# Performance work log

Hardware: AMD Instinct MI355X
Metric: run time of the kernel (lower is better)

The kernel has to match this reference:

```python
import jax, jax.numpy as jnp
import numpy as np

# SorscherRNN constants. NOTE: AdaptationRNN.__init__ swaps the names:
# self.beta = alpha_kwarg, self.alpha = beta_kwarg. We replicate the effective math:
#   z  = v_t @ W_ih.T + h @ W_hh.T - ALPHA_KW * v_adapt
#   v_adapt = v_adapt + BETA_KW * (z_prev - v_adapt)   (z_prev is the PREVIOUS post-subtraction z)
ALPHA_KW = 0.1  # used as the subtraction coefficient (self.beta)
BETA_KW = 0.9   # used as the adaptation rate (self.alpha)
NG, NP = 4096, 512
B, T = 64, 100


def setup_inputs() -> dict:
    key = jax.random.key(0)
    ks = jax.random.split(key, 6)
    def xavier(k, shape):
        fan_out, fan_in = shape
        a = jnp.sqrt(6.0 / (fan_in + fan_out))
        return jax.random.uniform(k, shape, jnp.float32, -a, a)
    return {
        "v": jax.random.normal(ks[0], (B, T, 2), jnp.float32),
        "p0": jax.random.uniform(ks[1], (B, NP), jnp.float32),
        "W_init": xavier(ks[2], (NG, NP)),  # init_position_encoder weight [Ng, Np]
        "W_ih": xavier(ks[3], (NG, 2)),     # RNN input weight W
        "W_hh": xavier(ks[4], (NG, NG)),    # RNN recurrent weight Wh
        "W_dec": xavier(ks[5], (NP, NG)),   # decoder weight [Np, Ng]
    }


def _sorscher_forward(v, p0, W_init, W_ih, W_hh, W_dec):
    h0 = p0 @ W_init.T                       # [B, Ng]
    va0 = jnp.zeros_like(h0)
    zp0 = jnp.zeros_like(h0)

    def step(carry, v_t):
        h, va, zp = carry
        z = v_t @ W_ih.T + h @ W_hh.T        # [B, Ng]
        z = z - ALPHA_KW * va                # z -= self.beta * v (old v)
        va = va + BETA_KW * (zp - va)        # v += self.alpha * (z_prev - v)
        s = jax.nn.relu(z)
        return (s, va, z), s                 # z_prev is post-subtraction z

    v_t_first = jnp.transpose(v, (1, 0, 2))  # [T, B, 2]
    _, g = jax.lax.scan(step, (h0, va0, zp0), v_t_first)
    g = jnp.transpose(g, (1, 0, 2))          # [B, T, Ng]
    return g @ W_dec.T                       # place_preds [B, T, Np] (log_softmax=False)


def reference(v, p0, W_init, W_ih, W_hh, W_dec):
    return _sorscher_forward(v, p0, W_init, W_ih, W_hh, W_dec)
```

## Files before the change

### kernel.cpp

```cpp
#include <hip/hip_runtime.h>
#include <hip/hip_bf16.h>

#define NG 4096
#define NP 512
#define TT 100
#define NCOL 4608
#define NKS 8

typedef __bf16  bf16x8 __attribute__((ext_vector_type(8)));
typedef float   f32x4  __attribute__((ext_vector_type(4)));
typedef __hip_bfloat16 bf;
typedef unsigned short u16;

#define ALPHA_BF 0.10009765625f
#define BETA_BF  0.8984375f

__device__ __forceinline__ bf16x8 ldfrag(const bf* p) {
  return *reinterpret_cast<const bf16x8*>(p);
}
__device__ __forceinline__ f32x4 mfma16(bf16x8 a, bf16x8 b, f32x4 c) {
  return __builtin_amdgcn_mfma_f32_16x16x32_bf16(a, b, c, 0, 0, 0);
}
__device__ __forceinline__ float ldin(const void* p, long i, int isf) {
  return isf ? ((const float*)p)[i] : __bfloat162float(((const bf*)p)[i]);
}
__device__ __forceinline__ float bfr(float x) {
  return __bfloat162float(__float2bfloat16(x));
}
__device__ __forceinline__ long qidx(int m, int c) {
  int kk = c >> 5, qd = (c >> 3) & 3, j = c & 7;
  int mt = m >> 4, lm = m & 15;
  return (((long)kk * 4 + mt) * 64 + (qd * 16 + lm)) * 8 + j;
}

__global__ void probe_kernel(const u16* __restrict__ w, int* __restrict__ flag) {
  int lane = threadIdx.x;
  int okall = 1, cntb = 0;
#pragma unroll
  for (int j = 0; j < 4; ++j) {
    u16 x = w[2 * (lane * 4 + j)];
    int e = (x >> 7) & 0xFF;
    int bok = (e >= 60 && e <= 126);
    int zok = (e == 0);
    okall &= (bok | zok);
    cntb += bok;
  }
  unsigned long long b1 = __ballot(okall != 0);
  unsigned long long b2 = __ballot(cntb >= 3);
  if (lane == 0)
    *flag = (b1 == ~0ull && __popcll(b2) >= 48) ? 0 : 1;
}

__global__ __launch_bounds__(256) void cvt_pack_kernel(
    const void* __restrict__ Whh, const void* __restrict__ Wdec,
    bf* __restrict__ PH, bf* __restrict__ PL,
    const int* __restrict__ flag) {
  int isf = *flag;
  long n = (long)NCOL * NG;
  long i = (long)blockIdx.x * 256 + threadIdx.x;
  long stride = (long)gridDim.x * 256;
  for (; i < n; i += stride) {
    int j    = (int)(i & 7);
    int lane = (int)((i >> 3) & 63);
    int kk   = (int)((i >> 9) & 127);
    int strip= (int)(i >> 16);
    int col  = strip * 16 + (lane & 15);
    int k    = kk * 32 + (lane >> 4) * 8 + j;
    long src = (col < NG) ? ((long)col * NG + k)
                          : ((long)(col - NG) * NG + k);
    const void* W = (col < NG) ? Whh : Wdec;
    float x = ldin(W, src, isf);
    bf h = __float2bfloat16(x);
    PH[i] = h;
    PL[i] = __float2bfloat16(isf ? (x - __bfloat162float(h)) : 0.f);
  }
}

__global__ __launch_bounds__(256) void init_kernel(
    const void* __restrict__ p0, const void* __restrict__ Winit,
    const int* __restrict__ flag,
    bf* __restrict__ hi0, bf* __restrict__ lo0,
    float* __restrict__ va, float* __restrict__ zp)
{
  int isf = *flag;
  int tid = blockIdx.x * 256 + threadIdx.x;
  int b = tid >> 12;
  int n = tid & 4095;
  float acc = 0.f;
  if (isf) {
    const float* pp = (const float*)p0 + (long)b * NP;
    const float* pw = (const float*)Winit + (long)n * NP;
#pragma unroll 4
    for (int k = 0; k < NP; k += 4) {
      float4 a = *(const float4*)(pp + k);
      float4 w = *(const float4*)(pw + k);
      acc += a.x * w.x + a.y * w.y + a.z * w.z + a.w * w.w;
    }
  } else {
    const bf* pp = (const bf*)p0 + (long)b * NP;
    const bf* pw = (const bf*)Winit + (long)n * NP;
#pragma unroll 4
    for (int k = 0; k < NP; k += 8) {
      bf16x8 a = ldfrag(pp + k);
      bf16x8 w = ldfrag(pw + k);
#pragma unroll
      for (int j = 0; j < 8; ++j) acc += (float)a[j] * (float)w[j];
    }
  }
  bf h = __float2bfloat16(acc);
  float lo = isf ? (acc - __bfloat162float(h)) : 0.f;
  long q = qidx(b, n);
  hi0[q] = h;
  lo0[q] = __float2bfloat16(lo);
  long idx = (long)b * NG + n;
  va[idx] = 0.f;
  zp[idx] = 0.f;
}

__global__ __launch_bounds__(256) void s1_kernel(
    const bf* __restrict__ Qh, const bf* __restrict__ Ql,
    float* __restrict__ part,
    const bf* __restrict__ PH, const bf* __restrict__ PL,
    const int* __restrict__ flag, int t)
{
  int ct = blockIdx.x >> 3;
  int ks = blockIdx.x & 7;
  bool isdec = (ct >= 64);
  if (isdec ? (t == 0) : (t == TT)) return;

  int isf = *flag;
  int tid  = threadIdx.x;
  int wave = tid >> 6;
  int lane = tid & 63;
  int quad = lane >> 4, l16 = lane & 15;
  int strip = ct * 4 + wave;

  const bf* pBh = PH + ((long)strip * 128 + ks * 16) * 512 + lane * 8;
  const bf* pBl = PL + ((long)strip * 128 + ks * 16) * 512 + lane * 8;
  const bf* pAh = Qh + (long)ks * 32768 + lane * 8;
  const bf* pAl = Ql + (long)ks * 32768 + lane * 8;

  f32x4 acc0 = {0.f,0.f,0.f,0.f}, acc1 = acc0, acc2 = acc0, acc3 = acc0;
  if (isf) {
#pragma unroll 4
    for (int i = 0; i < 16; ++i) {
      const bf* ah = pAh + i * 2048;
      const bf* al = pAl + i * 2048;
      bf16x8 bh = ldfrag(pBh + i * 512);
      bf16x8 bl = ldfrag(pBl + i * 512);
      bf16x8 a0 = ldfrag(ah);
      bf16x8 a1 = ldfrag(ah + 512);
      bf16x8 a2 = ldfrag(ah + 1024);
      bf16x8 a3 = ldfrag(ah + 1536);
      bf16x8 l0 = ldfrag(al);
      bf16x8 l1 = ldfrag(al + 512);
      bf16x8 l2 = ldfrag(al + 1024);
      bf16x8 l3 = ldfrag(al + 1536);
      acc0 = mfma16(a0, bh, acc0); acc0 = mfma16(l0, bh, acc0); acc0 = mfma16(a0, bl, acc0);
      acc1 = mfma16(a1, bh, acc1); acc1 = mfma16(l1, bh, acc1); acc1 = mfma16(a1, bl, acc1);
      acc2 = mfma16(a2, bh, acc2); acc2 = mfma16(l2, bh, acc2); acc2 = mfma16(a2, bl, acc2);
      acc3 = mfma16(a3, bh, acc3); acc3 = mfma16(l3, bh, acc3); acc3 = mfma16(a3, bl, acc3);
    }
  } else {
#pragma unroll 4
    for (int i = 0; i < 16; ++i) {
      const bf* ah = pAh + i * 2048;
      bf16x8 bh = ldfrag(pBh + i * 512);
      acc0 = mfma16(ldfrag(ah),        bh, acc0);
      acc1 = mfma16(ldfrag(ah + 512),  bh, acc1);
      acc2 = mfma16(ldfrag(ah + 1024), bh, acc2);
      acc3 = mfma16(ldfrag(ah + 1536), bh, acc3);
    }
  }

  float* pp = part + ((long)ks * 64 + quad * 4) * NCOL + strip * 16 + l16;
#pragma unroll
  for (int mt = 0; mt < 4; ++mt) {
    f32x4 a = (mt == 0) ? acc0 : (mt == 1) ? acc1 : (mt == 2) ? acc2 : acc3;
#pragma unroll
    for (int r = 0; r < 4; ++r)
      pp[((long)mt * 16 + r) * NCOL] = a[r];
  }
}

__global__ __launch_bounds__(256) void s2_kernel(
    const float* __restrict__ part,
    bf* __restrict__ hN, bf* __restrict__ lN,
    float* __restrict__ va, float* __restrict__ zp,
    const void* __restrict__ Wih, const void* __restrict__ v,
    const int* __restrict__ flag, void* __restrict__ out, int t)
{
  int isf = *flag;
#pragma unroll
  for (int i = 0; i < 4; ++i) {
    int e = blockIdx.x * 1024 + i * 256 + threadIdx.x;
    int m = e / NCOL;
    int c = e - m * NCOL;
    bool dcol = (c >= NG);
    if (dcol ? (t == 0) : (t == TT)) continue;

    float z = 0.f;
#pragma unroll
    for (int js = 0; js < NKS; ++js)
      z += part[((long)js * 64 + m) * NCOL + c];

    if (dcol) {
      long o = ((long)m * TT + (t - 1)) * NP + (c - NG);
      if (isf) ((float*)out)[o] = z;
      else     ((bf*)out)[o]    = __float2bfloat16(z);
      continue;
    }

    float w0 = ldin(Wih, 2L * c, isf);
    float w1 = ldin(Wih, 2L * c + 1, isf);
    float v0 = ldin(v, ((long)m * TT + t) * 2, isf);
    float v1 = ldin(v, ((long)m * TT + t) * 2 + 1, isf);

    long idx = (long)m * NG + c;
    float vao = va[idx], zpo = zp[idx];
    float s;
    if (isf) {
      z += v0 * w0 + v1 * w1;
      z -= 0.1f * vao;
      va[idx] = vao + 0.9f * (zpo - vao);
      zp[idx] = z;
      s = fmaxf(z, 0.f);
      bf sh = __float2bfloat16(s);
      long q = qidx(m, c);
      hN[q] = sh;
      lN[q] = __float2bfloat16(s - __bfloat162float(sh));
    } else {
      float zmm = bfr(z);
      float zv  = bfr(v0 * w0 + v1 * w1);
      float z0  = bfr(zmm + zv);
      float sub = bfr(ALPHA_BF * vao);
      float z1  = bfr(z0 - sub);
      float d   = bfr(zpo - vao);
      float mm  = bfr(BETA_BF * d);
      va[idx]   = bfr(vao + mm);
      zp[idx]   = z1;
      s = fmaxf(z1, 0.f);
      long q = qidx(m, c);
      hN[q] = __float2bfloat16(s);
      lN[q] = __float2bfloat16(0.f);
    }
  }
}

extern "C" void kernel_launch(void* const* d_in, const int* in_sizes, int n_in,
                              void* d_out, int out_size, void* d_ws, size_t ws_size,
                              hipStream_t stream) {
  const void* v     = d_in[0];
  const void* p0    = d_in[1];
  const void* Winit = d_in[2];
  const void* Wih   = d_in[3];
  const void* Whh   = d_in[4];
  const void* Wdec  = d_in[5];

  size_t off = 0;
  char* w = (char*)d_ws;
  int*   flag = (int*)(w + off);          off += 64;
  bf*    PH   = (bf*)(w + off);           off += (size_t)NCOL * NG * 2;
  bf*    PL   = (bf*)(w + off);           off += (size_t)NCOL * NG * 2;
  bf* hi0 = (bf*)(w + off);               off += (size_t)64 * NG * 2;
  bf* hi1 = (bf*)(w + off);               off += (size_t)64 * NG * 2;
  bf* lo0 = (bf*)(w + off);               off += (size_t)64 * NG * 2;
  bf* lo1 = (bf*)(w + off);               off += (size_t)64 * NG * 2;
  float* va   = (float*)(w + off);        off += (size_t)64 * NG * 4;
  float* zp   = (float*)(w + off);        off += (size_t)64 * NG * 4;
  float* part = (float*)(w + off);        off += (size_t)NKS * 64 * NCOL * 4;

  if (ws_size < off) return;

  probe_kernel<<<1, 64, 0, stream>>>((const u16*)Whh, flag);
  cvt_pack_kernel<<<8192, 256, 0, stream>>>(Whh, Wdec, PH, PL, flag);
  init_kernel<<<1024, 256, 0, stream>>>(p0, Winit, flag, hi0, lo0, va, zp);

  bf* hbuf[2] = { hi0, hi1 };
  bf* lbuf[2] = { lo0, lo1 };
  for (int t = 0; t <= TT; ++t) {
    s1_kernel<<<576, 256, 0, stream>>>(hbuf[t & 1], lbuf[t & 1], part,
                                       PH, PL, flag, t);
    s2_kernel<<<288, 256, 0, stream>>>(part, hbuf[(t + 1) & 1],
                                       lbuf[(t + 1) & 1], va, zp,
                                       Wih, v, flag, d_out, t);
  }
}
```

Baseline: 2.882 ms.

## Fuse split-K matmul and recurrence update into one kernel with LDS reduction

Merges the per-step s1 (split-K MFMA partial products to global memory) and s2 (reduction plus recurrence update) kernels into a single 512-thread kernel. Each block now handles one 16-column strip and half the batch, with 8 waves covering the K splits, and reduces the partials through shared memory instead of a global buffer. This halves the per-step launch count and removes the global partial-sum round trip, but each wave now computes only two M tiles, so B fragments are reused less. The weight packing kernel is also vectorised to 8 elements per thread, and the init GEMV is restructured to use wave-level shuffle reductions.

```diff
diff --git a/kernel.cpp b/kernel.cpp
--- a/kernel.cpp
+++ b/kernel.cpp
@@ -56,23 +56,35 @@
     bf* __restrict__ PH, bf* __restrict__ PL,
     const int* __restrict__ flag) {
   int isf = *flag;
-  long n = (long)NCOL * NG;
+  long n8 = (long)NCOL * NG / 8;
   long i = (long)blockIdx.x * 256 + threadIdx.x;
   long stride = (long)gridDim.x * 256;
-  for (; i < n; i += stride) {
-    int j    = (int)(i & 7);
-    int lane = (int)((i >> 3) & 63);
-    int kk   = (int)((i >> 9) & 127);
-    int strip= (int)(i >> 16);
+  for (; i < n8; i += stride) {
+    int lane = (int)(i & 63);
+    int kk   = (int)((i >> 6) & 127);
+    int strip= (int)(i >> 13);
     int col  = strip * 16 + (lane & 15);
-    int k    = kk * 32 + (lane >> 4) * 8 + j;
-    long src = (col < NG) ? ((long)col * NG + k)
-                          : ((long)(col - NG) * NG + k);
+    int k0   = kk * 32 + (lane >> 4) * 8;
     const void* W = (col < NG) ? Whh : Wdec;
-    float x = ldin(W, src, isf);
-    bf h = __float2bfloat16(x);
-    PH[i] = h;
-    PL[i] = __float2bfloat16(isf ? (x - __bfloat162float(h)) : 0.f);
+    long src = (long)((col < NG) ? col : col - NG) * NG + k0;
+    if (isf) {
+      const float* ps = (const float*)W + src;
+      float4 x = *(const float4*)ps, y = *(const float4*)(ps + 4);
+      float xs[8] = {x.x, x.y, x.z, x.w, y.x, y.y, y.z, y.w};
+      bf16x8 h, l;
+#pragma unroll
+      for (int j = 0; j < 8; ++j) {
+        bf hh = __float2bfloat16(xs[j]);
+        bf ll = __float2bfloat16(xs[j] - __bfloat162float(hh));
+        h[j] = *reinterpret_cast<__bf16*>(&hh);
+        l[j] = *reinterpret_cast<__bf16*>(&ll);
+      }
+      *reinterpret_cast<bf16x8*>(PH + i * 8) = h;
+      *reinterpret_cast<bf16x8*>(PL + i * 8) = l;
+    } else {
+      *reinterpret_cast<bf16x8*>(PH + i * 8) =
+          *reinterpret_cast<const bf16x8*>((const bf*)W + src);
+    }
   }
 }
 
@@ -83,166 +95,151 @@
     float* __restrict__ va, float* __restrict__ zp)
 {
   int isf = *flag;
-  int tid = blockIdx.x * 256 + threadIdx.x;
-  int b = tid >> 12;
-  int n = tid & 4095;
-  float acc = 0.f;
+  int g = blockIdx.x * 4 + (threadIdx.x >> 6);
+  int lane = threadIdx.x & 63;
+  int b  = g >> 7;
+  int n0 = g & 127;
+  float pf[8];
   if (isf) {
-    const float* pp = (const float*)p0 + (long)b * NP;
-    const float* pw = (const float*)Winit + (long)n * NP;
-#pragma unroll 4
-    for (int k = 0; k < NP; k += 4) {
-      float4 a = *(const float4*)(pp + k);
-      float4 w = *(const float4*)(pw + k);
-      acc += a.x * w.x + a.y * w.y + a.z * w.z + a.w * w.w;
-    }
+    const float* pp = (const float*)p0 + (long)b * NP + lane * 8;
+    float4 x = *(const float4*)pp, y = *(const float4*)(pp + 4);
+    pf[0]=x.x; pf[1]=x.y; pf[2]=x.z; pf[3]=x.w;
+    pf[4]=y.x; pf[5]=y.y; pf[6]=y.z; pf[7]=y.w;
   } else {
-    const bf* pp = (const bf*)p0 + (long)b * NP;
-    const bf* pw = (const bf*)Winit + (long)n * NP;
-#pragma unroll 4
-    for (int k = 0; k < NP; k += 8) {
-      bf16x8 a = ldfrag(pp + k);
-      bf16x8 w = ldfrag(pw + k);
-#pragma unroll
-      for (int j = 0; j < 8; ++j) acc += (float)a[j] * (float)w[j];
-    }
-  }
-  bf h = __float2bfloat16(acc);
-  float lo = isf ? (acc - __bfloat162float(h)) : 0.f;
-  long q = qidx(b, n);
-  hi0[q] = h;
-  lo0[q] = __float2bfloat16(lo);
-  long idx = (long)b * NG + n;
-  va[idx] = 0.f;
-  zp[idx] = 0.f;
-}
-
-__global__ __launch_bounds__(256) void s1_kernel(
+    bf16x8 a = ldfrag((const bf*)p0 + (long)b * NP + lane * 8);
+#pragma unroll
+    for (int j = 0; j < 8; ++j) pf[j] = (float)a[j];
+  }
+  for (int it = 0; it < 32; ++it) {
+    int n = n0 + (it << 7);
+    float acc;
+    if (isf) {
+      const float* pw = (const float*)Winit + (long)n * NP + lane * 8;
+      float4 x = *(const float4*)pw, y = *(const float4*)(pw + 4);
+      acc = pf[0]*x.x + pf[1]*x.y + pf[2]*x.z + pf[3]*x.w
+          + pf[4]*y.x + pf[5]*y.y + pf[6]*y.z + pf[7]*y.w;
+    } else {
+      bf16x8 wv = ldfrag((const bf*)Winit + (long)n * NP + lane * 8);
+      acc = 0.f;
+#pragma unroll
+      for (int j = 0; j < 8; ++j) acc += pf[j] * (float)wv[j];
+    }
+#pragma unroll
+    for (int s = 32; s >= 1; s >>= 1) acc += __shfl_xor(acc, s, 64);
+    if (lane == 0) {
+      bf h = __float2bfloat16(acc);
+      float lo = isf ? (acc - __bfloat162float(h)) : 0.f;
+      long q = qidx(b, n);
+      hi0[q] = h;
+      lo0[q] = __float2bfloat16(lo);
+      long idx = (long)b * NG + n;
+      va[idx] = 0.f;
+      zp[idx] = 0.f;
+    }
+  }
+}
+
+__global__ __launch_bounds__(512, 4) void s12_kernel(
     const bf* __restrict__ Qh, const bf* __restrict__ Ql,
-    float* __restrict__ part,
+    bf* __restrict__ hN, bf* __restrict__ lN,
+    float* __restrict__ va, float* __restrict__ zp,
     const bf* __restrict__ PH, const bf* __restrict__ PL,
-    const int* __restrict__ flag, int t)
+    const void* __restrict__ Wih, const void* __restrict__ vin,
+    const int* __restrict__ flag, void* __restrict__ out, int t)
 {
-  int ct = blockIdx.x >> 3;
-  int ks = blockIdx.x & 7;
-  bool isdec = (ct >= 64);
+  int strip = blockIdx.x >> 1;
+  int mh    = blockIdx.x & 1;
+  bool isdec = (strip >= 256);
   if (isdec ? (t == 0) : (t == TT)) return;
 
   int isf = *flag;
-  int tid  = threadIdx.x;
-  int wave = tid >> 6;
+  int tid = threadIdx.x;
+  int ks   = tid >> 6;
   int lane = tid & 63;
   int quad = lane >> 4, l16 = lane & 15;
-  int strip = ct * 4 + wave;
 
   const bf* pBh = PH + ((long)strip * 128 + ks * 16) * 512 + lane * 8;
-  const bf* pBl = PL + ((long)strip * 128 + ks * 16) * 512 + lane * 8;
-  const bf* pAh = Qh + (long)ks * 32768 + lane * 8;
-  const bf* pAl = Ql + (long)ks * 32768 + lane * 8;
-
-  f32x4 acc0 = {0.f,0.f,0.f,0.f}, acc1 = acc0, acc2 = acc0, acc3 = acc0;
+  const bf* pAh = Qh + (long)ks * 32768 + mh * 1024 + lane * 8;
+
+  f32x4 acc0 = {0.f,0.f,0.f,0.f}, acc1 = acc0;
   if (isf) {
+    const bf* pBl = PL + ((long)strip * 128 + ks * 16) * 512 + lane * 8;
+    const bf* pAl = Ql + (long)ks * 32768 + mh * 1024 + lane * 8;
 #pragma unroll 4
     for (int i = 0; i < 16; ++i) {
+      bf16x8 bh = ldfrag(pBh + i * 512);
+      bf16x8 bl = ldfrag(pBl + i * 512);
       const bf* ah = pAh + i * 2048;
       const bf* al = pAl + i * 2048;
-      bf16x8 bh = ldfrag(pBh + i * 512);
-      bf16x8 bl = ldfrag(pBl + i * 512);
-      bf16x8 a0 = ldfrag(ah);
-      bf16x8 a1 = ldfrag(ah + 512);
-      bf16x8 a2 = ldfrag(ah + 1024);
-      bf16x8 a3 = ldfrag(ah + 1536);
-      bf16x8 l0 = ldfrag(al);
-      bf16x8 l1 = ldfrag(al + 512);
-      bf16x8 l2 = ldfrag(al + 1024);
-      bf16x8 l3 = ldfrag(al + 1536);
+      bf16x8 a0 = ldfrag(ah),       a1 = ldfrag(ah + 512);
+      bf16x8 l0 = ldfrag(al),       l1 = ldfrag(al + 512);
       acc0 = mfma16(a0, bh, acc0); acc0 = mfma16(l0, bh, acc0); acc0 = mfma16(a0, bl, acc0);
       acc1 = mfma16(a1, bh, acc1); acc1 = mfma16(l1, bh, acc1); acc1 = mfma16(a1, bl, acc1);
-      acc2 = mfma16(a2, bh, acc2); acc2 = mfma16(l2, bh, acc2); acc2 = mfma16(a2, bl, acc2);
-      acc3 = mfma16(a3, bh, acc3); acc3 = mfma16(l3, bh, acc3); acc3 = mfma16(a3, bl, acc3);
     }
   } else {
 #pragma unroll 4
     for (int i = 0; i < 16; ++i) {
+      bf16x8 bh = ldfrag(pBh + i * 512);
       const bf* ah = pAh + i * 2048;
-      bf16x8 bh = ldfrag(pBh + i * 512);
-      acc0 = mfma16(ldfrag(ah),        bh, acc0);
-      acc1 = mfma16(ldfrag(ah + 512),  bh, acc1);
-      acc2 = mfma16(ldfrag(ah + 1024), bh, acc2);
-      acc3 = mfma16(ldfrag(ah + 1536), bh, acc3);
-    }
-  }
-
-  float* pp = part + ((long)ks * 64 + quad * 4) * NCOL + strip * 16 + l16;
-#pragma unroll
-  for (int mt = 0; mt < 4; ++mt) {
-    f32x4 a = (mt == 0) ? acc0 : (mt == 1) ? acc1 : (mt == 2) ? acc2 : acc3;
-#pragma unroll
-    for (int r = 0; r < 4; ++r)
-      pp[((long)mt * 16 + r) * NCOL] = a[r];
-  }
-}
-
-__global__ __launch_bounds__(256) void s2_kernel(
-    const float* __restrict__ part,
-    bf* __restrict__ hN, bf* __restrict__ lN,
-    float* __restrict__ va, float* __restrict__ zp,
-    const void* __restrict__ Wih, const void* __restrict__ v,
-    const int* __restrict__ flag, void* __restrict__ out, int t)
-{
-  int isf = *flag;
-#pragma unroll
-  for (int i = 0; i < 4; ++i) {
-    int e = blockIdx.x * 1024 + i * 256 + threadIdx.x;
-    int m = e / NCOL;
-    int c = e - m * NCOL;
-    bool dcol = (c >= NG);
-    if (dcol ? (t == 0) : (t == TT)) continue;
-
+      acc0 = mfma16(ldfrag(ah),       bh, acc0);
+      acc1 = mfma16(ldfrag(ah + 512), bh, acc1);
+    }
+  }
+
+  __shared__ float red[NKS][32][16];
+#pragma unroll
+  for (int r = 0; r < 4; ++r) {
+    red[ks][quad * 4 + r][l16]      = acc0[r];
+    red[ks][16 + quad * 4 + r][l16] = acc1[r];
+  }
+  __syncthreads();
+
+  {
+    int ml  = tid >> 4;
+    int c16 = tid & 15;
+    int m = mh * 32 + ml;
+    int c = strip * 16 + c16;
     float z = 0.f;
 #pragma unroll
-    for (int js = 0; js < NKS; ++js)
-      z += part[((long)js * 64 + m) * NCOL + c];
-
-    if (dcol) {
+    for (int k2 = 0; k2 < NKS; ++k2)
+      z += red[k2][ml][c16];
+
+    if (isdec) {
       long o = ((long)m * TT + (t - 1)) * NP + (c - NG);
       if (isf) ((float*)out)[o] = z;
       else     ((bf*)out)[o]    = __float2bfloat16(z);
-      continue;
-    }
-
-    float w0 = ldin(Wih, 2L * c, isf);
-    float w1 = ldin(Wih, 2L * c + 1, isf);
-    float v0 = ldin(v, ((long)m * TT + t) * 2, isf);
-    float v1 = ldin(v, ((long)m * TT + t) * 2 + 1, isf);
-
-    long idx = (long)m * NG + c;
-    float vao = va[idx], zpo = zp[idx];
-    float s;
-    if (isf) {
-      z += v0 * w0 + v1 * w1;
-      z -= 0.1f * vao;
-      va[idx] = vao + 0.9f * (zpo - vao);
-      zp[idx] = z;
-      s = fmaxf(z, 0.f);
-      bf sh = __float2bfloat16(s);
-      long q = qidx(m, c);
-      hN[q] = sh;
-      lN[q] = __float2bfloat16(s - __bfloat162float(sh));
     } else {
-      float zmm = bfr(z);
-      float zv  = bfr(v0 * w0 + v1 * w1);
-      float z0  = bfr(zmm + zv);
-      float sub = bfr(ALPHA_BF * vao);
-      float z1  = bfr(z0 - sub);
-      float d   = bfr(zpo - vao);
-      float mm  = bfr(BETA_BF * d);
-      va[idx]   = bfr(vao + mm);
-      zp[idx]   = z1;
-      s = fmaxf(z1, 0.f);
-      long q = qidx(m, c);
-      hN[q] = __float2bfloat16(s);
-      lN[q] = __float2bfloat16(0.f);
+      float w0 = ldin(Wih, 2L * c, isf);
+      float w1 = ldin(Wih, 2L * c + 1, isf);
+      float v0 = ldin(vin, ((long)m * TT + t) * 2, isf);
+      float v1 = ldin(vin, ((long)m * TT + t) * 2 + 1, isf);
+      long idx = (long)m * NG + c;
+      float vao = va[idx], zpo = zp[idx];
+      if (isf) {
+        z += v0 * w0 + v1 * w1;
+        z -= 0.1f * vao;
+        va[idx] = vao + 0.9f * (zpo - vao);
+        zp[idx] = z;
+        float s = fmaxf(z, 0.f);
+        bf sh = __float2bfloat16(s);
+        long q = qidx(m, c);
+        hN[q] = sh;
+        lN[q] = __float2bfloat16(s - __bfloat162float(sh));
+      } else {
+        float zmm = bfr(z);
+        float zv  = bfr(v0 * w0 + v1 * w1);
+        float z0  = bfr(zmm + zv);
+        float sub = bfr(ALPHA_BF * vao);
+        float z1  = bfr(z0 - sub);
+        float d   = bfr(zpo - vao);
+        float mm  = bfr(BETA_BF * d);
+        va[idx]   = bfr(vao + mm);
+        zp[idx]   = z1;
+        float s = fmaxf(z1, 0.f);
+        long q = qidx(m, c);
+        hN[q] = __float2bfloat16(s);
+        lN[q] = __float2bfloat16(0.f);
+      }
     }
   }
 }
@@ -268,21 +265,19 @@
   bf* lo1 = (bf*)(w + off);               off += (size_t)64 * NG * 2;
   float* va   = (float*)(w + off);        off += (size_t)64 * NG * 4;
   float* zp   = (float*)(w + off);        off += (size_t)64 * NG * 4;
-  float* part = (float*)(w + off);        off += (size_t)NKS * 64 * NCOL * 4;
 
   if (ws_size < off) return;
 
   probe_kernel<<<1, 64, 0, stream>>>((const u16*)Whh, flag);
-  cvt_pack_kernel<<<8192, 256, 0, stream>>>(Whh, Wdec, PH, PL, flag);
-  init_kernel<<<1024, 256, 0, stream>>>(p0, Winit, flag, hi0, lo0, va, zp);
+  cvt_pack_kernel<<<9216, 256, 0, stream>>>(Whh, Wdec, PH, PL, flag);
+  init_kernel<<<2048, 256, 0, stream>>>(p0, Winit, flag, hi0, lo0, va, zp);
 
   bf* hbuf[2] = { hi0, hi1 };
   bf* lbuf[2] = { lo0, lo1 };
   for (int t = 0; t <= TT; ++t) {
-    s1_kernel<<<576, 256, 0, stream>>>(hbuf[t & 1], lbuf[t & 1], part,
-                                       PH, PL, flag, t);
-    s2_kernel<<<288, 256, 0, stream>>>(part, hbuf[(t + 1) & 1],
-                                       lbuf[(t + 1) & 1], va, zp,
-                                       Wih, v, flag, d_out, t);
-  }
-}
+    s12_kernel<<<576, 512, 0, stream>>>(hbuf[t & 1], lbuf[t & 1],
+                                        hbuf[(t + 1) & 1], lbuf[(t + 1) & 1],
+                                        va, zp, PH, PL, Wih, v, flag,
+                                        d_out, t);
+  }
+}
```

Measured after the change: 3.432 ms. +19.1%, slower.
